# Kernel tuning notes

Hardware: AMD Instinct MI355X
Metric: run time of the kernel (lower is better)

The kernel has to match this reference:

```python
import jax, jax.numpy as jnp
import numpy as np

B, L, D = 8, 4096, 4096
E, R, K = 8, 16, 2
ALPHA = 1.0
EPS = 1e-5

def setup_inputs() -> dict:
    key = jax.random.key(0)
    ks = jax.random.split(key, 5)
    x = jax.random.normal(ks[0], (B, L, D), dtype=jnp.float32)
    gate_w = jax.random.normal(ks[1], (E, D), dtype=jnp.float32) * 0.02
    gate_b = jnp.zeros((E,), dtype=jnp.float32)
    A_w = jax.random.normal(ks[2], (E, R, D), dtype=jnp.float32) * 0.02
    B_w = jax.random.normal(ks[3], (E, D, R), dtype=jnp.float32) * 0.02
    gamma = jnp.ones((D,), dtype=jnp.float32)
    beta = jnp.zeros((D,), dtype=jnp.float32)
    return {"x": x, "gate_w": gate_w, "gate_b": gate_b, "A_w": A_w,
            "B_w": B_w, "gamma": gamma, "beta": beta}

def reference(x, gate_w, gate_b, A_w, B_w, gamma, beta):
    scale = ALPHA / R
    # pooled hidden state per sequence: [B, D]
    h = x.mean(axis=1)
    # router: gate logits -> top-k -> softmax over selected
    logits = h @ gate_w.T + gate_b                     # [B, E]
    top_vals, top_idx = jax.lax.top_k(logits, K)       # [B, K]
    w = jax.nn.softmax(top_vals, axis=-1)              # [B, K]
    # gather selected experts' LoRA factors
    A_sel = A_w[top_idx]                               # [B, K, R, D]
    B_sel = B_w[top_idx]                               # [B, K, D, R]
    z = jnp.einsum('bkrd,bd->bkr', A_sel, h)           # down-proj
    eo = jnp.einsum('bkdr,bkr->bkd', B_sel, z) * scale # up-proj
    delta = jnp.sum(w[..., None] * eo, axis=1)         # [B, D]
    # residual + LayerNorm (broadcast delta over seq dim)
    y = x + delta[:, None, :]
    mu = y.mean(axis=-1, keepdims=True)
    var = y.var(axis=-1, keepdims=True)
    return (y - mu) * jax.lax.rsqrt(var + EPS) * gamma + beta
```

## Files before the change

kernel.cpp:

```cpp
#include <hip/hip_runtime.h>

#define BB    8
#define LSEQ  4096
#define DD    4096
#define EE    8
#define RR    16
#define KK    2
#define NSLICE_MAX 128
#define LORA_SCALE (1.0f / 16.0f)
#define LN_EPS 1e-5f

typedef float f4 __attribute__((ext_vector_type(4)));

__device__ __forceinline__ float wave_sum(float v) {
#pragma unroll
    for (int off = 32; off > 0; off >>= 1)
        v += __shfl_xor(v, off, 64);
    return v;
}

__global__ __launch_bounds__(256) void colsum_kernel(
    const f4* __restrict__ x, f4* __restrict__ partial, int rows_per_slice)
{
    const int tid = threadIdx.x;
    const int b = blockIdx.x;
    const int sl = blockIdx.y;
    const size_t row0 = (size_t)b * LSEQ + (size_t)sl * rows_per_slice;
    const f4* p = x + row0 * (DD / 4);

    f4 acc[4];
#pragma unroll
    for (int i = 0; i < 4; ++i) acc[i] = (f4)(0.f);

#pragma unroll 2
    for (int l = 0; l < rows_per_slice; ++l) {
        const f4* pr = p + (size_t)l * (DD / 4);
#pragma unroll
        for (int i = 0; i < 4; ++i) {
            f4 xv = __builtin_nontemporal_load(&pr[tid + i * 256]);
            acc[i] += xv;
        }
    }
    f4* dst = partial + ((size_t)sl * BB + b) * (DD / 4);
#pragma unroll
    for (int i = 0; i < 4; ++i) dst[tid + i * 256] = acc[i];
}

__global__ __launch_bounds__(1024) void router_delta_kernel(
    const float* __restrict__ partial, int nslice,
    const float* __restrict__ gate_w, const float* __restrict__ gate_b,
    const float* __restrict__ A_w, const float* __restrict__ B_w,
    float* __restrict__ delta)
{
    __shared__ float hbuf[DD];
    __shared__ float redl[EE * 16];
    __shared__ float lgbuf[EE];
    __shared__ float redz[KK * RR * 16];
    __shared__ float zbuf[KK * RR];
    __shared__ int   sel[KK];
    __shared__ float wsel[KK];

    const int b = blockIdx.x;
    const int tid = threadIdx.x;
    const int lane = tid & 63;
    const int wid = tid >> 6;

    for (int d = tid; d < DD; d += 1024) {
        float s = 0.f;
#pragma unroll 8
        for (int sl = 0; sl < nslice; ++sl)
            s += partial[((size_t)sl * BB + b) * DD + d];
        hbuf[d] = s * (1.0f / LSEQ);
    }
    __syncthreads();

    float lacc[EE];
#pragma unroll
    for (int e = 0; e < EE; ++e) lacc[e] = 0.f;
    for (int d = tid; d < DD; d += 1024) {
        float hd = hbuf[d];
#pragma unroll
        for (int e = 0; e < EE; ++e) lacc[e] += hd * gate_w[e * DD + d];
    }
#pragma unroll
    for (int e = 0; e < EE; ++e) {
        float s = wave_sum(lacc[e]);
        if (lane == 0) redl[e * 16 + wid] = s;
    }
    __syncthreads();
    if (tid < EE) {
        float s = 0.f;
#pragma unroll
        for (int w = 0; w < 16; ++w) s += redl[tid * 16 + w];
        lgbuf[tid] = s + gate_b[tid];
    }
    __syncthreads();
    if (tid == 0) {
        int i0 = 0;
        for (int e = 1; e < EE; ++e) if (lgbuf[e] > lgbuf[i0]) i0 = e;
        int i1 = (i0 == 0) ? 1 : 0;
        for (int e = 0; e < EE; ++e) if (e != i0 && lgbuf[e] > lgbuf[i1]) i1 = e;
        float e1 = __expf(lgbuf[i1] - lgbuf[i0]);
        float inv = 1.0f / (1.0f + e1);
        sel[0] = i0; sel[1] = i1;
        wsel[0] = inv; wsel[1] = e1 * inv;
    }
    __syncthreads();

    float zacc[KK][RR];
#pragma unroll
    for (int k = 0; k < KK; ++k)
#pragma unroll
        for (int r = 0; r < RR; ++r) zacc[k][r] = 0.f;
    const float* A0 = A_w + (size_t)sel[0] * RR * DD;
    const float* A1 = A_w + (size_t)sel[1] * RR * DD;
    for (int d = tid; d < DD; d += 1024) {
        float hd = hbuf[d];
#pragma unroll
        for (int r = 0; r < RR; ++r) zacc[0][r] += hd * A0[r * DD + d];
#pragma unroll
        for (int r = 0; r < RR; ++r) zacc[1][r] += hd * A1[r * DD + d];
    }
#pragma unroll
    for (int k = 0; k < KK; ++k)
#pragma unroll
        for (int r = 0; r < RR; ++r) {
            float s = wave_sum(zacc[k][r]);
            if (lane == 0) redz[(k * RR + r) * 16 + wid] = s;
        }
    __syncthreads();
    if (tid < KK * RR) {
        float s = 0.f;
#pragma unroll
        for (int w = 0; w < 16; ++w) s += redz[tid * 16 + w];
        zbuf[tid] = s;
    }
    __syncthreads();

    const float w0 = wsel[0], w1 = wsel[1];
    const float* B0 = B_w + (size_t)sel[0] * DD * RR;
    const float* B1 = B_w + (size_t)sel[1] * DD * RR;
    for (int d = tid; d < DD; d += 1024) {
        float s0 = 0.f, s1 = 0.f;
#pragma unroll
        for (int r = 0; r < RR; ++r) {
            s0 += B0[d * RR + r] * zbuf[r];
            s1 += B1[d * RR + r] * zbuf[RR + r];
        }
        delta[(size_t)b * DD + d] = LORA_SCALE * (w0 * s0 + w1 * s1);
    }
}

__global__ __launch_bounds__(256) void resid_ln_kernel(
    const f4* __restrict__ x, const f4* __restrict__ delta,
    const f4* __restrict__ gamma, const f4* __restrict__ beta,
    f4* __restrict__ out)
{
    const int tid = threadIdx.x;
    const int lane = tid & 63, wid = tid >> 6;
    const int row = blockIdx.x * 4 + wid;
    const int b = row >> 12;
    const f4* xr = x + (size_t)row * (DD / 4);
    const f4* dr = delta + (size_t)b * (DD / 4);

    f4 v[16];
    float sum = 0.f, sq = 0.f;
#pragma unroll
    for (int i = 0; i < 16; ++i) {
        const int idx = lane + i * 64;
        f4 xv = __builtin_nontemporal_load(&xr[idx]);
        f4 dv = dr[idx];
        xv += dv;
        v[i] = xv;
        sum += xv.x + xv.y + xv.z + xv.w;
        sq  += xv.x * xv.x + xv.y * xv.y + xv.z * xv.z + xv.w * xv.w;
    }
    sum = wave_sum(sum);
    sq  = wave_sum(sq);
    const float mean = sum * (1.0f / DD);
    const float var  = sq * (1.0f / DD) - mean * mean;
    const float rstd = rsqrtf(var + LN_EPS);

    f4* orow = out + (size_t)row * (DD / 4);
#pragma unroll
    for (int i = 0; i < 16; ++i) {
        const int idx = lane + i * 64;
        f4 gv = gamma[idx];
        f4 bv = beta[idx];
        f4 xv = v[i];
        f4 o;
        o.x = (xv.x - mean) * rstd * gv.x + bv.x;
        o.y = (xv.y - mean) * rstd * gv.y + bv.y;
        o.z = (xv.z - mean) * rstd * gv.z + bv.z;
        o.w = (xv.w - mean) * rstd * gv.w + bv.w;
        __builtin_nontemporal_store(o, &orow[idx]);
    }
}

extern "C" void kernel_launch(void* const* d_in, const int* in_sizes, int n_in,
                              void* d_out, int out_size, void* d_ws, size_t ws_size,
                              hipStream_t stream) {
    const float* x      = (const float*)d_in[0];
    const float* gate_w = (const float*)d_in[1];
    const float* gate_b = (const float*)d_in[2];
    const float* A_w    = (const float*)d_in[3];
    const float* B_w    = (const float*)d_in[4];
    const float* gamma  = (const float*)d_in[5];
    const float* beta   = (const float*)d_in[6];
    float* out = (float*)d_out;
    float* ws  = (float*)d_ws;

    const size_t bd = (size_t)BB * DD;
    int nslice = NSLICE_MAX;
    while (nslice > 1 && (size_t)(nslice + 1) * bd * sizeof(float) > ws_size)
        nslice >>= 1;
    float* partial = ws;
    float* delta   = ws + (size_t)nslice * bd;

    dim3 g1(BB, nslice);
    colsum_kernel<<<g1, 256, 0, stream>>>(
        (const f4*)x, (f4*)partial, LSEQ / nslice);

    router_delta_kernel<<<BB, 1024, 0, stream>>>(
        partial, nslice, gate_w, gate_b, A_w, B_w, delta);

    resid_ln_kernel<<<BB * LSEQ / 4, 256, 0, stream>>>(
        (const f4*)x, (const f4*)delta,
        (const f4*)gamma, (const f4*)beta, (f4*)out);
}
```

Baseline: 377.1 us.

## Use cached loads, batch-major colsum grid, vectorize router with f4

```diff
diff --git a/kernel.cpp b/kernel.cpp
--- a/kernel.cpp
+++ b/kernel.cpp
@@ -6,7 +6,7 @@
 #define EE    8
 #define RR    16
 #define KK    2
-#define NSLICE_MAX 128
+#define NSLICE 128
 #define LORA_SCALE (1.0f / 16.0f)
 #define LN_EPS 1e-5f
 
@@ -17,14 +17,19 @@
     for (int off = 32; off > 0; off >>= 1)
         v += __shfl_xor(v, off, 64);
     return v;
+}
+
+__device__ __forceinline__ float dot4(f4 a, f4 b) {
+    return a.x * b.x + a.y * b.y + a.z * b.z + a.w * b.w;
 }
 
 __global__ __launch_bounds__(256) void colsum_kernel(
     const f4* __restrict__ x, f4* __restrict__ partial, int rows_per_slice)
 {
     const int tid = threadIdx.x;
-    const int b = blockIdx.x;
-    const int sl = blockIdx.y;
+    const int bid = blockIdx.x;
+    const int b  = bid >> 7;
+    const int sl = bid & (NSLICE - 1);
     const size_t row0 = (size_t)b * LSEQ + (size_t)sl * rows_per_slice;
     const f4* p = x + row0 * (DD / 4);
 
@@ -36,10 +41,8 @@
     for (int l = 0; l < rows_per_slice; ++l) {
         const f4* pr = p + (size_t)l * (DD / 4);
 #pragma unroll
-        for (int i = 0; i < 4; ++i) {
-            f4 xv = __builtin_nontemporal_load(&pr[tid + i * 256]);
-            acc[i] += xv;
-        }
+        for (int i = 0; i < 4; ++i)
+            acc[i] += pr[tid + i * 256];
     }
     f4* dst = partial + ((size_t)sl * BB + b) * (DD / 4);
 #pragma unroll
@@ -47,12 +50,11 @@
 }
 
 __global__ __launch_bounds__(1024) void router_delta_kernel(
-    const float* __restrict__ partial, int nslice,
-    const float* __restrict__ gate_w, const float* __restrict__ gate_b,
-    const float* __restrict__ A_w, const float* __restrict__ B_w,
-    float* __restrict__ delta)
+    const f4* __restrict__ partial, int nslice,
+    const f4* __restrict__ gate_w, const float* __restrict__ gate_b,
+    const f4* __restrict__ A_w, const f4* __restrict__ B_w,
+    f4* __restrict__ delta)
 {
-    __shared__ float hbuf[DD];
     __shared__ float redl[EE * 16];
     __shared__ float lgbuf[EE];
     __shared__ float redz[KK * RR * 16];
@@ -65,26 +67,15 @@
     const int lane = tid & 63;
     const int wid = tid >> 6;
 
-    for (int d = tid; d < DD; d += 1024) {
-        float s = 0.f;
+    f4 acc = (f4)(0.f);
 #pragma unroll 8
-        for (int sl = 0; sl < nslice; ++sl)
-            s += partial[((size_t)sl * BB + b) * DD + d];
-        hbuf[d] = s * (1.0f / LSEQ);
-    }
-    __syncthreads();
-
-    float lacc[EE];
-#pragma unroll
-    for (int e = 0; e < EE; ++e) lacc[e] = 0.f;
-    for (int d = tid; d < DD; d += 1024) {
-        float hd = hbuf[d];
-#pragma unroll
-        for (int e = 0; e < EE; ++e) lacc[e] += hd * gate_w[e * DD + d];
-    }
+    for (int sl = 0; sl < nslice; ++sl)
+        acc += partial[((size_t)sl * BB + b) * (DD / 4) + tid];
+    const f4 h = acc * (1.0f / LSEQ);
+
 #pragma unroll
     for (int e = 0; e < EE; ++e) {
-        float s = wave_sum(lacc[e]);
+        float s = wave_sum(dot4(h, gate_w[e * (DD / 4) + tid]));
         if (lane == 0) redl[e * 16 + wid] = s;
     }
     __syncthreads();
@@ -107,27 +98,17 @@
     }
     __syncthreads();
 
-    float zacc[KK][RR];
-#pragma unroll
-    for (int k = 0; k < KK; ++k)
-#pragma unroll
-        for (int r = 0; r < RR; ++r) zacc[k][r] = 0.f;
-    const float* A0 = A_w + (size_t)sel[0] * RR * DD;
-    const float* A1 = A_w + (size_t)sel[1] * RR * DD;
-    for (int d = tid; d < DD; d += 1024) {
-        float hd = hbuf[d];
-#pragma unroll
-        for (int r = 0; r < RR; ++r) zacc[0][r] += hd * A0[r * DD + d];
-#pragma unroll
-        for (int r = 0; r < RR; ++r) zacc[1][r] += hd * A1[r * DD + d];
-    }
-#pragma unroll
-    for (int k = 0; k < KK; ++k)
-#pragma unroll
-        for (int r = 0; r < RR; ++r) {
-            float s = wave_sum(zacc[k][r]);
-            if (lane == 0) redz[(k * RR + r) * 16 + wid] = s;
+    const f4* A0 = A_w + (size_t)sel[0] * RR * (DD / 4);
+    const f4* A1 = A_w + (size_t)sel[1] * RR * (DD / 4);
+#pragma unroll
+    for (int r = 0; r < RR; ++r) {
+        float s0 = wave_sum(dot4(h, A0[r * (DD / 4) + tid]));
+        float s1 = wave_sum(dot4(h, A1[r * (DD / 4) + tid]));
+        if (lane == 0) {
+            redz[r * 16 + wid] = s0;
+            redz[(RR + r) * 16 + wid] = s1;
         }
+    }
     __syncthreads();
     if (tid < KK * RR) {
         float s = 0.f;
@@ -138,17 +119,26 @@
     __syncthreads();
 
     const float w0 = wsel[0], w1 = wsel[1];
-    const float* B0 = B_w + (size_t)sel[0] * DD * RR;
-    const float* B1 = B_w + (size_t)sel[1] * DD * RR;
-    for (int d = tid; d < DD; d += 1024) {
+    const f4* B0 = B_w + (size_t)sel[0] * DD * (RR / 4);
+    const f4* B1 = B_w + (size_t)sel[1] * DD * (RR / 4);
+    f4 o;
+#pragma unroll
+    for (int c = 0; c < 4; ++c) {
+        const int d = tid * 4 + c;
         float s0 = 0.f, s1 = 0.f;
 #pragma unroll
-        for (int r = 0; r < RR; ++r) {
-            s0 += B0[d * RR + r] * zbuf[r];
-            s1 += B1[d * RR + r] * zbuf[RR + r];
+        for (int rv = 0; rv < RR / 4; ++rv) {
+            f4 b0 = B0[d * (RR / 4) + rv];
+            f4 b1 = B1[d * (RR / 4) + rv];
+            s0 += b0.x * zbuf[rv * 4] + b0.y * zbuf[rv * 4 + 1]
+                + b0.z * zbuf[rv * 4 + 2] + b0.w * zbuf[rv * 4 + 3];
+            s1 += b1.x * zbuf[RR + rv * 4] + b1.y * zbuf[RR + rv * 4 + 1]
+                + b1.z * zbuf[RR + rv * 4 + 2] + b1.w * zbuf[RR + rv * 4 + 3];
         }
-        delta[(size_t)b * DD + d] = LORA_SCALE * (w0 * s0 + w1 * s1);
-    }
+        float v = LORA_SCALE * (w0 * s0 + w1 * s1);
+        if (c == 0) o.x = v; else if (c == 1) o.y = v; else if (c == 2) o.z = v; else o.w = v;
+    }
+    delta[(size_t)b * (DD / 4) + tid] = o;
 }
 
 __global__ __launch_bounds__(256) void resid_ln_kernel(
@@ -168,7 +158,7 @@
 #pragma unroll
     for (int i = 0; i < 16; ++i) {
         const int idx = lane + i * 64;
-        f4 xv = __builtin_nontemporal_load(&xr[idx]);
+        f4 xv = xr[idx];
         f4 dv = dr[idx];
         xv += dv;
         v[i] = xv;
@@ -193,7 +183,7 @@
         o.y = (xv.y - mean) * rstd * gv.y + bv.y;
         o.z = (xv.z - mean) * rstd * gv.z + bv.z;
         o.w = (xv.w - mean) * rstd * gv.w + bv.w;
-        __builtin_nontemporal_store(o, &orow[idx]);
+        orow[idx] = o;
     }
 }
 
@@ -210,19 +200,15 @@
     float* out = (float*)d_out;
     float* ws  = (float*)d_ws;
 
-    const size_t bd = (size_t)BB * DD;
-    int nslice = NSLICE_MAX;
-    while (nslice > 1 && (size_t)(nslice + 1) * bd * sizeof(float) > ws_size)
-        nslice >>= 1;
     float* partial = ws;
-    float* delta   = ws + (size_t)nslice * bd;
-
-    dim3 g1(BB, nslice);
-    colsum_kernel<<<g1, 256, 0, stream>>>(
-        (const f4*)x, (f4*)partial, LSEQ / nslice);
+    float* delta   = ws + (size_t)NSLICE * BB * DD;
+
+    colsum_kernel<<<BB * NSLICE, 256, 0, stream>>>(
+        (const f4*)x, (f4*)partial, LSEQ / NSLICE);
 
     router_delta_kernel<<<BB, 1024, 0, stream>>>(
-        partial, nslice, gate_w, gate_b, A_w, B_w, delta);
+        (const f4*)partial, NSLICE, (const f4*)gate_w, gate_b,
+        (const f4*)A_w, (const f4*)B_w, (f4*)delta);
 
     resid_ln_kernel<<<BB * LSEQ / 4, 256, 0, stream>>>(
         (const f4*)x, (const f4*)delta,
```

Result: slower. 405.0 us (+7.4%).
